# Optimization experiments

Hardware: AMD Instinct MI355X
Metric: run time of the kernel (lower is better)

## Reference

```python
import jax, jax.numpy as jnp
import numpy as np

B, Q, K, H = 16, 512, 512, 64
DQ, DK, DV = 256, 256, 256
MASK_VAL = -1000000.0


def setup_inputs() -> dict:
    key = jax.random.key(0)
    ks = jax.random.split(key, 7)
    queries = jax.random.normal(ks[0], (B, Q, DQ), dtype=jnp.float32)
    keys = jax.random.normal(ks[1], (B, K, DK), dtype=jnp.float32)
    values = jax.random.normal(ks[2], (B, K, DV), dtype=jnp.float32)
    valid_lens = jax.random.randint(ks[3], (B,), 1, K + 1).astype(jnp.int32)
    # learned params (nn.Linear, bias=False): weight shape [out, in]
    Wq = jax.random.normal(ks[4], (H, DQ), dtype=jnp.float32) / np.sqrt(DQ)
    Wk = jax.random.normal(ks[5], (H, DK), dtype=jnp.float32) / np.sqrt(DK)
    wv = jax.random.normal(ks[6], (H,), dtype=jnp.float32) / np.sqrt(H)
    return {"queries": queries, "keys": keys, "values": values,
            "valid_lens": valid_lens, "Wq": Wq, "Wk": Wk, "wv": wv}


def reference(queries, keys, values, valid_lens, Wq, Wk, wv):
    q = jnp.einsum('bqd,hd->bqh', queries, Wq)          # [B,Q,H]
    k = jnp.einsum('bkd,hd->bkh', keys, Wk)             # [B,K,H]
    feats = jnp.tanh(q[:, :, None, :] + k[:, None, :, :])  # [B,Q,K,H]
    scores = jnp.einsum('bqkh,h->bqk', feats, wv)       # [B,Q,K]
    kmask = jnp.arange(K)[None, None, :] < valid_lens[:, None, None]
    scores = jnp.where(kmask, scores, MASK_VAL)
    attn = jax.nn.softmax(scores, axis=-1)              # [B,Q,K]
    return jnp.einsum('bqk,bkv->bqv', attn, values)     # [B,Q,DV]
```

## Files before the change

### kernel.cpp

```cpp
#include <hip/hip_runtime.h>
#include <math.h>

#if defined(__has_builtin)
#  if __has_builtin(__builtin_amdgcn_exp2f)
#    define EXP2F(x) __builtin_amdgcn_exp2f(x)
#  endif
#  if __has_builtin(__builtin_amdgcn_rcpf)
#    define RCPF(x) __builtin_amdgcn_rcpf(x)
#  endif
#endif
#ifndef EXP2F
#  define EXP2F(x) exp2f(x)
#endif
#ifndef RCPF
#  define RCPF(x) (1.0f/(x))
#endif

static constexpr int Bn = 16, QN = 512, KN = 512, Hn = 64, DV = 256, DIN = 256;
static constexpr int TQ = 8;
static constexpr float TWO_LOG2E = 2.8853900817779268f;
static constexpr float LOG2E     = 1.4426950408889634f;

typedef __attribute__((ext_vector_type(8))) short short8;
typedef __attribute__((ext_vector_type(4))) float f32x4;

__device__ __forceinline__ short f2bf(float x) {
  unsigned u = __builtin_bit_cast(unsigned, x);
  u += 0x7FFF + ((u >> 16) & 1);
  return (short)(u >> 16);
}
__device__ __forceinline__ float bf2f(short h) {
  return __builtin_bit_cast(float, ((unsigned)(unsigned short)h) << 16);
}

__global__ __launch_bounds__(256) void prep_kernel(
    const float* __restrict__ Wq, const float* __restrict__ Wk,
    ushort* __restrict__ wqh, ushort* __restrict__ wql,
    ushort* __restrict__ wkh, ushort* __restrict__ wkl)
{
  int i = blockIdx.x * 256 + threadIdx.x;
  float xq = Wq[i];
  short hq = f2bf(xq);
  wqh[i] = (ushort)hq; wql[i] = (ushort)f2bf(xq - bf2f(hq));
  float xk = Wk[i];
  short hk = f2bf(xk);
  wkh[i] = (ushort)hk; wkl[i] = (ushort)f2bf(xk - bf2f(hk));
}

__global__ __launch_bounds__(256) void proj_mfma(
    const float* __restrict__ queries, const float* __restrict__ keys,
    const ushort* __restrict__ wqh, const ushort* __restrict__ wql,
    const ushort* __restrict__ wkh, const ushort* __restrict__ wkl,
    float* __restrict__ qe, float* __restrict__ ekT)
{
  __shared__ float tr[4][16][20];
  int t = threadIdx.x;
  int lane = t & 63, wid = t >> 6;
  bool is_k = blockIdx.x >= 512;
  int trow = (blockIdx.x & 511) * 16;
  const float*  X  = is_k ? keys : queries;
  const ushort* Wh = is_k ? wkh : wqh;
  const ushort* Wl = is_k ? wkl : wql;
  int mr = lane & 15, quad = lane >> 4;
  const float*  xp  = X  + (size_t)(trow + mr) * DIN + quad * 8;
  const ushort* whp = Wh + (size_t)(wid * 16 + mr) * DIN + quad * 8;
  const ushort* wlp = Wl + (size_t)(wid * 16 + mr) * DIN + quad * 8;

  f32x4 acc = (f32x4){0.f, 0.f, 0.f, 0.f};
  #pragma unroll
  for (int kc = 0; kc < 8; ++kc) {
    float4 a0 = *(const float4*)(xp + kc * 32);
    float4 a1 = *(const float4*)(xp + kc * 32 + 4);
    float av[8] = {a0.x, a0.y, a0.z, a0.w, a1.x, a1.y, a1.z, a1.w};
    short8 ah, al;
    #pragma unroll
    for (int j = 0; j < 8; ++j) {
      ah[j] = f2bf(av[j]);
      al[j] = f2bf(av[j] - bf2f(ah[j]));
    }
    short8 bh = *(const short8*)(whp + kc * 32);
    short8 bl = *(const short8*)(wlp + kc * 32);
    acc = __builtin_amdgcn_mfma_f32_16x16x32_bf16(al, bh, acc, 0, 0, 0);
    acc = __builtin_amdgcn_mfma_f32_16x16x32_bf16(ah, bl, acc, 0, 0, 0);
    acc = __builtin_amdgcn_mfma_f32_16x16x32_bf16(ah, bh, acc, 0, 0, 0);
  }
  if (!is_k) {
    #pragma unroll
    for (int reg = 0; reg < 4; ++reg) {
      int row = trow + quad * 4 + reg;
      qe[(size_t)row * Hn + wid * 16 + mr] = EXP2F(acc[reg] * TWO_LOG2E);
    }
  } else {
    #pragma unroll
    for (int reg = 0; reg < 4; ++reg)
      tr[wid][mr][quad * 4 + reg] = EXP2F(acc[reg] * TWO_LOG2E);
    int b = trow >> 9, kr = trow & (KN - 1);
    #pragma unroll
    for (int hp = 0; hp < 4; ++hp) {
      int h_l = hp * 4 + quad, k_l = mr;
      ekT[((size_t)b * Hn + wid * 16 + h_l) * KN + kr + k_l] = tr[wid][h_l][k_l];
    }
  }
}

__global__ __launch_bounds__(512) void attn_kernel(
    const float* __restrict__ qe,
    const float* __restrict__ ekT,
    const float* __restrict__ values,
    const int*   __restrict__ valid_lens,
    const float* __restrict__ wv,
    float* __restrict__ out)
{
  __shared__ __align__(16) float qes2[Hn][TQ];
  __shared__ __align__(16) float pt[KN][12];
  __shared__ __align__(16) float pacc[TQ][DV];
  __shared__ float wsum[8][TQ];
  __shared__ float inv_s[TQ];
  __shared__ int srank[Bn];

  int t = threadIdx.x;
  int lane = t & 63, wave = t >> 6;

  if (t < Bn) {
    int Lb = valid_lens[t];
    int r = 0;
    #pragma unroll
    for (int b2 = 0; b2 < Bn; ++b2) {
      int L2 = valid_lens[b2];
      r += (L2 > Lb || (L2 == Lb && b2 < t)) ? 1 : 0;
    }
    srank[r] = t;
  }
  __syncthreads();

  int cu = blockIdx.x & 255, slot = blockIdx.x >> 8;
  int m = cu >> 4;
  int jr = (slot == 0) ? m
         : (slot == 1) ? 15 - m
         : (slot == 2) ? ((m + 8) & 15)
                       : 15 - ((m + 8) & 15);
  int b = srank[jr];
  int q0 = (slot * 16 + (cu & 15)) * TQ;
  int L = valid_lens[b];

  qes2[t >> 3][t & 7] = qe[(size_t)(b * QN + q0 + (t & 7)) * Hn + (t >> 3)];
  __syncthreads();

  float S = 0.f;
  #pragma unroll
  for (int h = 0; h < Hn; ++h) S += wv[h];

  {
    int k = t;
    float p[TQ];
    if (k < L) {
      float sc[TQ];
      #pragma unroll
      for (int r = 0; r < TQ; ++r) sc[r] = S;
      const float* kb = ekT + (size_t)b * Hn * KN + k;
      for (int h0 = 0; h0 < Hn; h0 += 8) {
        float ekv[8];
        #pragma unroll
        for (int j = 0; j < 8; ++j)
          ekv[j] = kb[(size_t)(h0 + j) * KN];
        #pragma unroll
        for (int jp = 0; jp < 4; ++jp) {
          int ha = h0 + 2 * jp;
          float wa = 2.0f * wv[ha], wb = 2.0f * wv[ha + 1];
          float eka = ekv[2 * jp], ekb = ekv[2 * jp + 1];
          float4 qa0 = *(const float4*)&qes2[ha][0];
          float4 qa1 = *(const float4*)&qes2[ha][4];
          float4 qb0 = *(const float4*)&qes2[ha + 1][0];
          float4 qb1 = *(const float4*)&qes2[ha + 1][4];
          float da, db, num;
          da = qa0.x * eka + 1.0f; db = qb0.x * ekb + 1.0f;
          num = wa * db + wb * da; sc[0] -= num * RCPF(da * db);
          da = qa0.y * eka + 1.0f; db = qb0.y * ekb + 1.0f;
          num = wa * db + wb * da; sc[1] -= num * RCPF(da * db);
          da = qa0.z * eka + 1.0f; db = qb0.z * ekb + 1.0f;
          num = wa * db + wb * da; sc[2] -= num * RCPF(da * db);
          da = qa0.w * eka + 1.0f; db = qb0.w * ekb + 1.0f;
          num = wa * db + wb * da; sc[3] -= num * RCPF(da * db);
          da = qa1.x * eka + 1.0f; db = qb1.x * ekb + 1.0f;
          num = wa * db + wb * da; sc[4] -= num * RCPF(da * db);
          da = qa1.y * eka + 1.0f; db = qb1.y * ekb + 1.0f;
          num = wa * db + wb * da; sc[5] -= num * RCPF(da * db);
          da = qa1.z * eka + 1.0f; db = qb1.z * ekb + 1.0f;
          num = wa * db + wb * da; sc[6] -= num * RCPF(da * db);
          da = qa1.w * eka + 1.0f; db = qb1.w * ekb + 1.0f;
          num = wa * db + wb * da; sc[7] -= num * RCPF(da * db);
        }
      }
      #pragma unroll
      for (int r = 0; r < TQ; ++r) p[r] = EXP2F(sc[r] * LOG2E);
      *(float4*)&pt[k][0] = make_float4(p[0], p[1], p[2], p[3]);
      *(float4*)&pt[k][4] = make_float4(p[4], p[5], p[6], p[7]);
    } else {
      #pragma unroll
      for (int r = 0; r < TQ; ++r) p[r] = 0.f;
    }
    #pragma unroll
    for (int r = 0; r < TQ; ++r) {
      float s = p[r];
      #pragma unroll
      for (int off = 32; off > 0; off >>= 1) s += __shfl_xor(s, off, 64);
      if (lane == r) wsum[wave][r] = s;
    }
  }
  __syncthreads();
  if (t < TQ) {
    float s = 0.f;
    #pragma unroll
    for (int w = 0; w < 8; ++w) s += wsum[w][t];
    inv_s[t] = 1.0f / s;
  }

  int c = t & (DV - 1), half = t >> 8;
  int mid = L >> 1;
  int k0 = half ? mid : 0;
  int k1 = half ? L : mid;
  float acc[TQ];
  #pragma unroll
  for (int r = 0; r < TQ; ++r) acc[r] = 0.f;
  const float* vb = values + (size_t)b * KN * DV + c;
  #pragma unroll 4
  for (int k = k0; k < k1; ++k) {
    float val = vb[(size_t)k * DV];
    float4 pa = *(const float4*)&pt[k][0];
    float4 pb = *(const float4*)&pt[k][4];
    acc[0] += pa.x * val; acc[1] += pa.y * val;
    acc[2] += pa.z * val; acc[3] += pa.w * val;
    acc[4] += pb.x * val; acc[5] += pb.y * val;
    acc[6] += pb.z * val; acc[7] += pb.w * val;
  }
  if (half) {
    #pragma unroll
    for (int r = 0; r < TQ; ++r) pacc[r][c] = acc[r];
  }
  __syncthreads();
  if (!half) {
    float* ob = out + (size_t)(b * QN + q0) * DV + c;
    #pragma unroll
    for (int r = 0; r < TQ; ++r)
      ob[(size_t)r * DV] = (acc[r] + pacc[r][c]) * inv_s[r];
  }
}

extern "C" void kernel_launch(void* const* d_in, const int* in_sizes, int n_in,
                              void* d_out, int out_size, void* d_ws, size_t ws_size,
                              hipStream_t stream) {
  const float* queries    = (const float*)d_in[0];
  const float* keys       = (const float*)d_in[1];
  const float* values     = (const float*)d_in[2];
  const int*   valid_lens = (const int*)d_in[3];
  const float* Wq         = (const float*)d_in[4];
  const float* Wk         = (const float*)d_in[5];
  const float* wv         = (const float*)d_in[6];
  float* out = (float*)d_out;

  char* ws = (char*)d_ws;
  float*  qe  = (float*)ws;
  float*  ekT = qe + (size_t)Bn * QN * Hn;
  ushort* wqh = (ushort*)(ekT + (size_t)Bn * Hn * KN);
  ushort* wql = wqh + Hn * DIN;
  ushort* wkh = wql + Hn * DIN;
  ushort* wkl = wkh + Hn * DIN;

  prep_kernel<<<64, 256, 0, stream>>>(Wq, Wk, wqh, wql, wkh, wkl);
  proj_mfma<<<1024, 256, 0, stream>>>(queries, keys, wqh, wql, wkh, wkl, qe, ekT);
  attn_kernel<<<Bn * (QN / TQ), 512, 0, stream>>>(qe, ekT, values,
                                                  valid_lens, wv, out);
}
```

Before: 149.4 us.

## Halve query tile, drop weight prep kernel, and read transposed q from global

Removes the separate weight-splitting kernel by converting Wq/Wk to hi/lo bf16 inline in the projection kernel. Query projections are now written transposed like keys and read directly from global memory instead of being staged in shared memory. The query tile per block shrinks from 8 to 4, doubling the grid, and blocks are scheduled simply by length rank instead of the interleaved CU balancing scheme. The risks are that each ekT read and each values load is now reused across only half as many queries, so global traffic roughly doubles, and the load-balancing schedule is lost.

```diff
diff --git a/kernel.cpp b/kernel.cpp
--- a/kernel.cpp
+++ b/kernel.cpp
@@ -17,7 +17,7 @@
 #endif
 
 static constexpr int Bn = 16, QN = 512, KN = 512, Hn = 64, DV = 256, DIN = 256;
-static constexpr int TQ = 8;
+static constexpr int TQ = 4;
 static constexpr float TWO_LOG2E = 2.8853900817779268f;
 static constexpr float LOG2E     = 1.4426950408889634f;
 
@@ -33,86 +33,66 @@
   return __builtin_bit_cast(float, ((unsigned)(unsigned short)h) << 16);
 }
 
-__global__ __launch_bounds__(256) void prep_kernel(
-    const float* __restrict__ Wq, const float* __restrict__ Wk,
-    ushort* __restrict__ wqh, ushort* __restrict__ wql,
-    ushort* __restrict__ wkh, ushort* __restrict__ wkl)
-{
-  int i = blockIdx.x * 256 + threadIdx.x;
-  float xq = Wq[i];
-  short hq = f2bf(xq);
-  wqh[i] = (ushort)hq; wql[i] = (ushort)f2bf(xq - bf2f(hq));
-  float xk = Wk[i];
-  short hk = f2bf(xk);
-  wkh[i] = (ushort)hk; wkl[i] = (ushort)f2bf(xk - bf2f(hk));
-}
-
 __global__ __launch_bounds__(256) void proj_mfma(
     const float* __restrict__ queries, const float* __restrict__ keys,
-    const ushort* __restrict__ wqh, const ushort* __restrict__ wql,
-    const ushort* __restrict__ wkh, const ushort* __restrict__ wkl,
-    float* __restrict__ qe, float* __restrict__ ekT)
+    const float* __restrict__ Wq, const float* __restrict__ Wk,
+    const float* __restrict__ wv,
+    float* __restrict__ qT, float* __restrict__ ekT, float* __restrict__ wv2)
 {
   __shared__ float tr[4][16][20];
   int t = threadIdx.x;
   int lane = t & 63, wid = t >> 6;
+  if (blockIdx.x == 0 && t < Hn) wv2[t] = 2.0f * wv[t];
   bool is_k = blockIdx.x >= 512;
   int trow = (blockIdx.x & 511) * 16;
-  const float*  X  = is_k ? keys : queries;
-  const ushort* Wh = is_k ? wkh : wqh;
-  const ushort* Wl = is_k ? wkl : wql;
+  const float* X = is_k ? keys : queries;
+  const float* W = is_k ? Wk : Wq;
+  float* dT = is_k ? ekT : qT;
   int mr = lane & 15, quad = lane >> 4;
-  const float*  xp  = X  + (size_t)(trow + mr) * DIN + quad * 8;
-  const ushort* whp = Wh + (size_t)(wid * 16 + mr) * DIN + quad * 8;
-  const ushort* wlp = Wl + (size_t)(wid * 16 + mr) * DIN + quad * 8;
+  const float* xp = X + (size_t)(trow + mr) * DIN + quad * 8;
+  const float* wp = W + (size_t)(wid * 16 + mr) * DIN + quad * 8;
 
   f32x4 acc = (f32x4){0.f, 0.f, 0.f, 0.f};
   #pragma unroll
   for (int kc = 0; kc < 8; ++kc) {
     float4 a0 = *(const float4*)(xp + kc * 32);
     float4 a1 = *(const float4*)(xp + kc * 32 + 4);
+    float4 b0 = *(const float4*)(wp + kc * 32);
+    float4 b1 = *(const float4*)(wp + kc * 32 + 4);
     float av[8] = {a0.x, a0.y, a0.z, a0.w, a1.x, a1.y, a1.z, a1.w};
-    short8 ah, al;
+    float bv[8] = {b0.x, b0.y, b0.z, b0.w, b1.x, b1.y, b1.z, b1.w};
+    short8 ah, al, bh, bl;
     #pragma unroll
     for (int j = 0; j < 8; ++j) {
       ah[j] = f2bf(av[j]);
       al[j] = f2bf(av[j] - bf2f(ah[j]));
-    }
-    short8 bh = *(const short8*)(whp + kc * 32);
-    short8 bl = *(const short8*)(wlp + kc * 32);
+      bh[j] = f2bf(bv[j]);
+      bl[j] = f2bf(bv[j] - bf2f(bh[j]));
+    }
     acc = __builtin_amdgcn_mfma_f32_16x16x32_bf16(al, bh, acc, 0, 0, 0);
     acc = __builtin_amdgcn_mfma_f32_16x16x32_bf16(ah, bl, acc, 0, 0, 0);
     acc = __builtin_amdgcn_mfma_f32_16x16x32_bf16(ah, bh, acc, 0, 0, 0);
   }
-  if (!is_k) {
-    #pragma unroll
-    for (int reg = 0; reg < 4; ++reg) {
-      int row = trow + quad * 4 + reg;
-      qe[(size_t)row * Hn + wid * 16 + mr] = EXP2F(acc[reg] * TWO_LOG2E);
-    }
-  } else {
-    #pragma unroll
-    for (int reg = 0; reg < 4; ++reg)
-      tr[wid][mr][quad * 4 + reg] = EXP2F(acc[reg] * TWO_LOG2E);
-    int b = trow >> 9, kr = trow & (KN - 1);
-    #pragma unroll
-    for (int hp = 0; hp < 4; ++hp) {
-      int h_l = hp * 4 + quad, k_l = mr;
-      ekT[((size_t)b * Hn + wid * 16 + h_l) * KN + kr + k_l] = tr[wid][h_l][k_l];
-    }
+  #pragma unroll
+  for (int reg = 0; reg < 4; ++reg)
+    tr[wid][mr][quad * 4 + reg] = EXP2F(acc[reg] * TWO_LOG2E);
+  int b = trow >> 9, rr = trow & 511;
+  #pragma unroll
+  for (int hp = 0; hp < 4; ++hp) {
+    int h_l = hp * 4 + quad, r_l = mr;
+    dT[((size_t)b * Hn + wid * 16 + h_l) * 512 + rr + r_l] = tr[wid][h_l][r_l];
   }
 }
 
 __global__ __launch_bounds__(512) void attn_kernel(
-    const float* __restrict__ qe,
+    const float* __restrict__ qT,
     const float* __restrict__ ekT,
     const float* __restrict__ values,
     const int*   __restrict__ valid_lens,
-    const float* __restrict__ wv,
+    const float* __restrict__ wv2,
     float* __restrict__ out)
 {
-  __shared__ __align__(16) float qes2[Hn][TQ];
-  __shared__ __align__(16) float pt[KN][12];
+  __shared__ __align__(16) float pt[KN][TQ];
   __shared__ __align__(16) float pacc[TQ][DV];
   __shared__ float wsum[8][TQ];
   __shared__ float inv_s[TQ];
@@ -133,22 +113,15 @@
   }
   __syncthreads();
 
-  int cu = blockIdx.x & 255, slot = blockIdx.x >> 8;
-  int m = cu >> 4;
-  int jr = (slot == 0) ? m
-         : (slot == 1) ? 15 - m
-         : (slot == 2) ? ((m + 8) & 15)
-                       : 15 - ((m + 8) & 15);
-  int b = srank[jr];
-  int q0 = (slot * 16 + (cu & 15)) * TQ;
-  int L = valid_lens[b];
-
-  qes2[t >> 3][t & 7] = qe[(size_t)(b * QN + q0 + (t & 7)) * Hn + (t >> 3)];
-  __syncthreads();
+  int rank = blockIdx.x >> 7;
+  int b = __builtin_amdgcn_readfirstlane(srank[rank]);
+  int L = __builtin_amdgcn_readfirstlane(valid_lens[b]);
+  int q0 = (blockIdx.x & 127) * TQ;
 
   float S = 0.f;
   #pragma unroll
-  for (int h = 0; h < Hn; ++h) S += wv[h];
+  for (int h = 0; h < Hn; ++h) S += wv2[h];
+  S *= 0.5f;
 
   {
     int k = t;
@@ -158,6 +131,7 @@
       #pragma unroll
       for (int r = 0; r < TQ; ++r) sc[r] = S;
       const float* kb = ekT + (size_t)b * Hn * KN + k;
+      const float* qb = qT  + (size_t)b * Hn * QN + q0;
       for (int h0 = 0; h0 < Hn; h0 += 8) {
         float ekv[8];
         #pragma unroll
@@ -166,35 +140,24 @@
         #pragma unroll
         for (int jp = 0; jp < 4; ++jp) {
           int ha = h0 + 2 * jp;
-          float wa = 2.0f * wv[ha], wb = 2.0f * wv[ha + 1];
+          float wa = wv2[ha], wb = wv2[ha + 1];
+          float4 qa = *(const float4*)(qb + (size_t)ha * QN);
+          float4 qc = *(const float4*)(qb + (size_t)(ha + 1) * QN);
           float eka = ekv[2 * jp], ekb = ekv[2 * jp + 1];
-          float4 qa0 = *(const float4*)&qes2[ha][0];
-          float4 qa1 = *(const float4*)&qes2[ha][4];
-          float4 qb0 = *(const float4*)&qes2[ha + 1][0];
-          float4 qb1 = *(const float4*)&qes2[ha + 1][4];
           float da, db, num;
-          da = qa0.x * eka + 1.0f; db = qb0.x * ekb + 1.0f;
+          da = qa.x * eka + 1.0f; db = qc.x * ekb + 1.0f;
           num = wa * db + wb * da; sc[0] -= num * RCPF(da * db);
-          da = qa0.y * eka + 1.0f; db = qb0.y * ekb + 1.0f;
+          da = qa.y * eka + 1.0f; db = qc.y * ekb + 1.0f;
           num = wa * db + wb * da; sc[1] -= num * RCPF(da * db);
-          da = qa0.z * eka + 1.0f; db = qb0.z * ekb + 1.0f;
+          da = qa.z * eka + 1.0f; db = qc.z * ekb + 1.0f;
           num = wa * db + wb * da; sc[2] -= num * RCPF(da * db);
-          da = qa0.w * eka + 1.0f; db = qb0.w * ekb + 1.0f;
+          da = qa.w * eka + 1.0f; db = qc.w * ekb + 1.0f;
           num = wa * db + wb * da; sc[3] -= num * RCPF(da * db);
-          da = qa1.x * eka + 1.0f; db = qb1.x * ekb + 1.0f;
-          num = wa * db + wb * da; sc[4] -= num * RCPF(da * db);
-          da = qa1.y * eka + 1.0f; db = qb1.y * ekb + 1.0f;
-          num = wa * db + wb * da; sc[5] -= num * RCPF(da * db);
-          da = qa1.z * eka + 1.0f; db = qb1.z * ekb + 1.0f;
-          num = wa * db + wb * da; sc[6] -= num * RCPF(da * db);
-          da = qa1.w * eka + 1.0f; db = qb1.w * ekb + 1.0f;
-          num = wa * db + wb * da; sc[7] -= num * RCPF(da * db);
         }
       }
       #pragma unroll
       for (int r = 0; r < TQ; ++r) p[r] = EXP2F(sc[r] * LOG2E);
       *(float4*)&pt[k][0] = make_float4(p[0], p[1], p[2], p[3]);
-      *(float4*)&pt[k][4] = make_float4(p[4], p[5], p[6], p[7]);
     } else {
       #pragma unroll
       for (int r = 0; r < TQ; ++r) p[r] = 0.f;
@@ -219,19 +182,14 @@
   int mid = L >> 1;
   int k0 = half ? mid : 0;
   int k1 = half ? L : mid;
-  float acc[TQ];
-  #pragma unroll
-  for (int r = 0; r < TQ; ++r) acc[r] = 0.f;
+  float acc[TQ] = {0.f, 0.f, 0.f, 0.f};
   const float* vb = values + (size_t)b * KN * DV + c;
   #pragma unroll 4
   for (int k = k0; k < k1; ++k) {
     float val = vb[(size_t)k * DV];
     float4 pa = *(const float4*)&pt[k][0];
-    float4 pb = *(const float4*)&pt[k][4];
     acc[0] += pa.x * val; acc[1] += pa.y * val;
     acc[2] += pa.z * val; acc[3] += pa.w * val;
-    acc[4] += pb.x * val; acc[5] += pb.y * val;
-    acc[6] += pb.z * val; acc[7] += pb.w * val;
   }
   if (half) {
     #pragma unroll
@@ -259,15 +217,11 @@
   float* out = (float*)d_out;
 
   char* ws = (char*)d_ws;
-  float*  qe  = (float*)ws;
-  float*  ekT = qe + (size_t)Bn * QN * Hn;
-  ushort* wqh = (ushort*)(ekT + (size_t)Bn * Hn * KN);
-  ushort* wql = wqh + Hn * DIN;
-  ushort* wkh = wql + Hn * DIN;
-  ushort* wkl = wkh + Hn * DIN;
-
-  prep_kernel<<<64, 256, 0, stream>>>(Wq, Wk, wqh, wql, wkh, wkl);
-  proj_mfma<<<1024, 256, 0, stream>>>(queries, keys, wqh, wql, wkh, wkl, qe, ekT);
-  attn_kernel<<<Bn * (QN / TQ), 512, 0, stream>>>(qe, ekT, values,
-                                                  valid_lens, wv, out);
-}
+  float* qT  = (float*)ws;
+  float* ekT = qT + (size_t)Bn * Hn * QN;
+  float* wv2 = ekT + (size_t)Bn * Hn * KN;
+
+  proj_mfma<<<1024, 256, 0, stream>>>(queries, keys, Wq, Wk, wv, qT, ekT, wv2);
+  attn_kernel<<<Bn * (QN / TQ), 512, 0, stream>>>(qT, ekT, values,
+                                                  valid_lens, wv2, out);
+}
```

Measured after the change: 143.9 us. 1.04x faster.
